# Optimization experiments

Hardware: AMD Instinct MI355X
Metric: run time of the kernel (lower is better)

## Reference

```python
import jax, jax.numpy as jnp
import numpy as np

B, NQ, N, D, H, R = 8, 64, 257, 768, 6, 64
DH = D // H  # 128
ALL_Q_MID = NQ * R  # 4096
LN_EPS = 1e-5


def setup_inputs() -> dict:
    key = jax.random.key(0)
    ks = jax.random.split(key, 7)
    s = 0.02
    return {
        "x": jax.random.normal(ks[0], (B, NQ, D), jnp.float32),
        "context": jax.random.normal(ks[1], (B, N, D), jnp.float32),
        "Wq": jax.random.normal(ks[2], (D, D), jnp.float32) * s,
        "Wk": jax.random.normal(ks[3], (D, D), jnp.float32) * s,
        "Wv1": jax.random.normal(ks[4], (ALL_Q_MID, D), jnp.float32) * s,
        "ln_g": jnp.ones((ALL_Q_MID,), jnp.float32),
        "ln_b": jnp.zeros((ALL_Q_MID,), jnp.float32),
        "Wconv": jax.random.normal(ks[5], (NQ, D, R), jnp.float32) * s,
        "Wout": jax.random.normal(ks[6], (D, D), jnp.float32) * s,
    }


def reference(x, context, Wq, Wk, Wv1, ln_g, ln_b, Wconv, Wout):
    b, nq, d = x.shape
    n = context.shape[1]
    dh = d // H

    # q, k projections, split heads: (b, h, len, dh)
    q = (x @ Wq.T).reshape(b, nq, H, dh).transpose(0, 2, 1, 3)
    k = (context @ Wk.T).reshape(b, n, H, dh).transpose(0, 2, 1, 3)

    # q-aware V: Linear -> LayerNorm(all_q_mid) -> grouped 1x1 conv (per-query lora expand)
    mid = context @ Wv1.T                                   # (b, n, NQ*R)
    mu = mid.mean(-1, keepdims=True)
    var = mid.var(-1, keepdims=True)
    mid = (mid - mu) * jax.lax.rsqrt(var + LN_EPS) * ln_g + ln_b
    midq = mid.reshape(b, n, NQ, -1)                        # (b, n, Q, r)
    v = jnp.einsum('bnqr,qdr->bqnd', midq, Wconv)           # per-query V: (b, Q, n, d)
    v = v.reshape(b, NQ, n, H, dh).transpose(0, 3, 1, 2, 4)  # (b, h, Q, n, dh)

    scale = dh ** (-0.25)
    sim = jnp.einsum('bhid,bhjd->bhij', q * scale, k * scale)  # (b, h, Q, n)
    attn = jax.nn.softmax(sim, axis=-1)
    # per-query value aggregation: attn[i, j] pairs with v[i, j, :]
    out = jnp.einsum('bhij,bhijd->bhid', attn, v)           # (b, h, Q, dh)
    out = out.transpose(0, 2, 1, 3).reshape(b, nq, d)       # (b, Q, d)
    return out @ Wout.T
```

## Files before the change

kernel.cpp:

```cpp
#include <hip/hip_runtime.h>

#define DEV __device__ __forceinline__

typedef __attribute__((ext_vector_type(8))) short sv8;
typedef __attribute__((ext_vector_type(4))) short sv4;
typedef __attribute__((ext_vector_type(4))) float f32x4;

DEV short f2bf(float f) {
  unsigned u = __float_as_uint(f);
  unsigned r = (u + 0x7fffu + ((u >> 16) & 1u)) >> 16;
  return (short)r;
}
DEV float bf2f(short s) {
  return __uint_as_float(((unsigned)(unsigned short)s) << 16);
}

DEV void gload16(const void* g, void* l) {
  __builtin_amdgcn_global_load_lds((const __attribute__((address_space(1))) void*)g,
                                   (__attribute__((address_space(3))) void*)l, 16, 0, 0);
}

struct CvtArgs {
  const float* s0; const float* s1; const float* s2;
  const float* s3; const float* s4; const float* s5;
  short* d0; short* d1; short* d2; short* d3; short* d4; short* d5;
  int e0, e1, e2, e3, e4, e5;
};
__global__ __launch_bounds__(256) void cvt_all(CvtArgs a) {
  int i = blockIdx.x * 256 + threadIdx.x;
  if (i >= a.e5) return;
  const float* s; short* d; int base;
  if      (i < a.e0) { s = a.s0; d = a.d0; base = 0; }
  else if (i < a.e1) { s = a.s1; d = a.d1; base = a.e0; }
  else if (i < a.e2) { s = a.s2; d = a.d2; base = a.e1; }
  else if (i < a.e3) { s = a.s3; d = a.d3; base = a.e2; }
  else if (i < a.e4) { s = a.s4; d = a.d4; base = a.e3; }
  else               { s = a.s5; d = a.d5; base = a.e4; }
  int j = i - base;
  float4 v = ((const float4*)s)[j];
  sv4 o = { f2bf(v.x), f2bf(v.y), f2bf(v.z), f2bf(v.w) };
  ((sv4*)d)[j] = o;
}

template <int OUT_BF16>
DEV void gemm_tile(const short* __restrict__ A, const short* __restrict__ B,
                   void* __restrict__ C, int M, int N, int K, int bm, int bn) {
  __shared__ __align__(16) short As[128 * 32];
  __shared__ __align__(16) short Bs[128 * 32];
  const int tid = threadIdx.x;
  const int wave = tid >> 6, lane = tid & 63;
  const int wr = wave >> 1, wc = wave & 1;
  const int row0 = bm * 128, col0 = bn * 128;
  const int rsel = lane & 15, koff = (lane >> 4) * 8;
  const int Am = M - 1, Bm = N - 1;
  const int lr = lane >> 2, c8 = (lane & 3) * 8;

  const f32x4 z = {0.f, 0.f, 0.f, 0.f};
  f32x4 acc[4][4];
#pragma unroll
  for (int m = 0; m < 4; ++m)
#pragma unroll
    for (int n = 0; n < 4; ++n) acc[m][n] = z;

  for (int k0 = 0; k0 < K; k0 += 32) {
#pragma unroll
    for (int s = 0; s < 2; ++s) {
      int chunk = s * 4 + wave;
      int rr = chunk * 16 + lr;
      int gr = row0 + rr; if (gr > Am) gr = Am;
      gload16(A + (size_t)gr * K + k0 + c8, As + chunk * 512);
      int gc = col0 + rr; if (gc > Bm) gc = Bm;
      gload16(B + (size_t)gc * K + k0 + c8, Bs + chunk * 512);
    }
    __syncthreads();
    sv8 a[4], b[4];
#pragma unroll
    for (int m = 0; m < 4; ++m) a[m] = *(const sv8*)(As + (wr * 64 + m * 16 + rsel) * 32 + koff);
#pragma unroll
    for (int n = 0; n < 4; ++n) b[n] = *(const sv8*)(Bs + (wc * 64 + n * 16 + rsel) * 32 + koff);
#pragma unroll
    for (int m = 0; m < 4; ++m)
#pragma unroll
      for (int n = 0; n < 4; ++n)
        acc[m][n] = __builtin_amdgcn_mfma_f32_16x16x32_bf16(a[m], b[n], acc[m][n], 0, 0, 0);
    __syncthreads();
  }

  const int cc = lane & 15, cr = (lane >> 4) * 4;
#pragma unroll
  for (int m = 0; m < 4; ++m)
#pragma unroll
    for (int n = 0; n < 4; ++n) {
      int c = col0 + wc * 64 + n * 16 + cc;
#pragma unroll
      for (int j = 0; j < 4; ++j) {
        int r = row0 + wr * 64 + m * 16 + cr + j;
        if (r < M && c < N) {
          float v = acc[m][n][j];
          if (OUT_BF16) ((short*)C)[(size_t)r * N + c] = f2bf(v);
          else          ((float*)C)[(size_t)r * N + c] = v;
        }
      }
    }
}

struct GSeg { const short* A; const short* B; short* C; int M; int nb; int blk0; };
__global__ __launch_bounds__(256) void gemm3(GSeg g0, GSeg g1, GSeg g2) {
  int bid = blockIdx.x;
  GSeg g;
  if (bid < g1.blk0) g = g0;
  else if (bid < g2.blk0) g = g1;
  else g = g2;
  int local = bid - g.blk0;
  int bm = local / g.nb, bn = local % g.nb;
  gemm_tile<1>(g.A, g.B, g.C, g.M, g.nb * 128, 768, bm, bn);
}

__global__ __launch_bounds__(256) void gemm_out_k(const short* __restrict__ A,
                                                  const short* __restrict__ B,
                                                  float* __restrict__ C) {
  gemm_tile<0>(A, B, C, 512, 768, 768, blockIdx.x, blockIdx.y);
}

DEV void ln_body(int row, short* __restrict__ mid, const float* __restrict__ g,
                 const float* __restrict__ bb, float* rs, float* rss) {
  short* p = mid + (size_t)row * 4096;
  const int tid = threadIdx.x;
  sv8 v0 = *(const sv8*)(p + tid * 16);
  sv8 v1 = *(const sv8*)(p + tid * 16 + 8);
  float x[16];
#pragma unroll
  for (int j = 0; j < 8; ++j) { x[j] = bf2f(v0[j]); x[8 + j] = bf2f(v1[j]); }
  float s = 0.f, ss = 0.f;
#pragma unroll
  for (int j = 0; j < 16; ++j) { s += x[j]; ss += x[j] * x[j]; }
#pragma unroll
  for (int off = 32; off; off >>= 1) { s += __shfl_xor(s, off); ss += __shfl_xor(ss, off); }
  if ((tid & 63) == 0) { rs[tid >> 6] = s; rss[tid >> 6] = ss; }
  __syncthreads();
  float S = rs[0] + rs[1] + rs[2] + rs[3];
  float SS = rss[0] + rss[1] + rss[2] + rss[3];
  const float inv_n = 1.0f / 4096.0f;
  float mu = S * inv_n;
  float var = SS * inv_n - mu * mu;
  float rstd = rsqrtf(var + 1e-5f);
  const float4* g4 = (const float4*)(g + tid * 16);
  const float4* b4 = (const float4*)(bb + tid * 16);
  float y[16];
#pragma unroll
  for (int i = 0; i < 4; ++i) {
    float4 gg = g4[i], bv = b4[i];
    y[i * 4 + 0] = (x[i * 4 + 0] - mu) * rstd * gg.x + bv.x;
    y[i * 4 + 1] = (x[i * 4 + 1] - mu) * rstd * gg.y + bv.y;
    y[i * 4 + 2] = (x[i * 4 + 2] - mu) * rstd * gg.z + bv.z;
    y[i * 4 + 3] = (x[i * 4 + 3] - mu) * rstd * gg.w + bv.w;
  }
  sv8 o0, o1;
#pragma unroll
  for (int j = 0; j < 8; ++j) { o0[j] = f2bf(y[j]); o1[j] = f2bf(y[8 + j]); }
  *(sv8*)(p + tid * 16) = o0;
  *(sv8*)(p + tid * 16 + 8) = o1;
}

DEV void attn_body(int bh, const short* __restrict__ qb, const short* __restrict__ kb,
                   float* __restrict__ attn, float (*wred)[64]) {
  const int b = bh / 6, h = bh % 6;
  const int tid = threadIdx.x, wave = tid >> 6, lane = tid & 63;
  const int rsel = lane & 15, koff = (lane >> 4) * 8;
  const int rhi = (lane >> 4) * 4;

  const f32x4 z = {0.f, 0.f, 0.f, 0.f};
  f32x4 acc[4][5];
#pragma unroll
  for (int m = 0; m < 4; ++m)
#pragma unroll
    for (int i = 0; i < 5; ++i) acc[m][i] = z;

#pragma unroll
  for (int k0 = 0; k0 < 128; k0 += 32) {
    sv8 a[4];
#pragma unroll
    for (int m = 0; m < 4; ++m)
      a[m] = *(const sv8*)(qb + (size_t)(b * 64 + m * 16 + rsel) * 768 + h * 128 + k0 + koff);
#pragma unroll
    for (int i = 0; i < 5; ++i) {
      int nf = wave + i * 4;
      if (nf > 16) continue;
      int j = nf * 16 + rsel; if (j > 256) j = 256;
      sv8 bf = *(const sv8*)(kb + (size_t)(b * 257 + j) * 768 + h * 128 + k0 + koff);
#pragma unroll
      for (int m = 0; m < 4; ++m)
        acc[m][i] = __builtin_amdgcn_mfma_f32_16x16x32_bf16(a[m], bf, acc[m][i], 0, 0, 0);
    }
  }
  const float S2 = 0.08838834764831845f;
#pragma unroll
  for (int m = 0; m < 4; ++m)
#pragma unroll
    for (int i = 0; i < 5; ++i) {
      int col = (wave + i * 4) * 16 + rsel;
      bool valid = col < 257;
#pragma unroll
      for (int j = 0; j < 4; ++j)
        acc[m][i][j] = valid ? acc[m][i][j] * S2 : -1e30f;
    }
  float mx[4][4];
#pragma unroll
  for (int m = 0; m < 4; ++m)
#pragma unroll
    for (int j = 0; j < 4; ++j) {
      float pm = acc[m][0][j];
#pragma unroll
      for (int i = 1; i < 5; ++i) pm = fmaxf(pm, acc[m][i][j]);
      pm = fmaxf(pm, __shfl_xor(pm, 1));
      pm = fmaxf(pm, __shfl_xor(pm, 2));
      pm = fmaxf(pm, __shfl_xor(pm, 4));
      pm = fmaxf(pm, __shfl_xor(pm, 8));
      mx[m][j] = pm;
      if (rsel == 0) wred[wave][m * 16 + rhi + j] = pm;
    }
  __syncthreads();
#pragma unroll
  for (int m = 0; m < 4; ++m)
#pragma unroll
    for (int j = 0; j < 4; ++j) {
      int row = m * 16 + rhi + j;
      mx[m][j] = fmaxf(fmaxf(wred[0][row], wred[1][row]), fmaxf(wred[2][row], wred[3][row]));
    }
  __syncthreads();
  float inv[4][4];
#pragma unroll
  for (int m = 0; m < 4; ++m)
#pragma unroll
    for (int j = 0; j < 4; ++j) {
      float ps = 0.f;
#pragma unroll
      for (int i = 0; i < 5; ++i) {
        float e = __expf(acc[m][i][j] - mx[m][j]);
        acc[m][i][j] = e;
        ps += e;
      }
      ps += __shfl_xor(ps, 1);
      ps += __shfl_xor(ps, 2);
      ps += __shfl_xor(ps, 4);
      ps += __shfl_xor(ps, 8);
      if (rsel == 0) wred[wave][m * 16 + rhi + j] = ps;
    }
  __syncthreads();
  float* base = attn + (size_t)bh * 64 * 257;
#pragma unroll
  for (int m = 0; m < 4; ++m)
#pragma unroll
    for (int j = 0; j < 4; ++j) {
      int row = m * 16 + rhi + j;
      float tot = wred[0][row] + wred[1][row] + wred[2][row] + wred[3][row];
      inv[m][j] = 1.f / tot;
    }
#pragma unroll
  for (int m = 0; m < 4; ++m)
#pragma unroll
    for (int i = 0; i < 5; ++i) {
      int nf = wave + i * 4;
      if (nf > 16) continue;
      int col = nf * 16 + rsel;
      if (col < 257) {
#pragma unroll
        for (int j = 0; j < 4; ++j)
          base[(size_t)(m * 16 + rhi + j) * 257 + col] = acc[m][i][j] * inv[m][j];
      }
    }
}

__global__ __launch_bounds__(256) void ln_attn(short* __restrict__ mid,
                                               const float* __restrict__ g,
                                               const float* __restrict__ bb,
                                               const short* __restrict__ qb,
                                               const short* __restrict__ kb,
                                               float* __restrict__ attn) {
  __shared__ float wred[4][64];
  __shared__ float rs[4], rss[4];
  if (blockIdx.x < 48) attn_body(blockIdx.x, qb, kb, attn, wred);
  else                 ln_body(blockIdx.x - 48, mid, g, bb, rs, rss);
}

__global__ __launch_bounds__(256) void tk_kernel(const float* __restrict__ attn,
                                                 const short* __restrict__ mid,
                                                 float* __restrict__ t) {
  const int bq = blockIdx.x;
  const int b = bq >> 6, q = bq & 63;
  const int tid = threadIdx.x;
  __shared__ short ms[257][64];
  __shared__ float as_[6][257];
  for (int lin = tid; lin < 257 * 8; lin += 256) {
    int j = lin >> 3, seg = (lin & 7) * 8;
    *(sv8*)(&ms[j][seg]) = *(const sv8*)(mid + (size_t)(b * 257 + j) * 4096 + q * 64 + seg);
  }
#pragma unroll
  for (int h = 0; h < 6; ++h)
    for (int j = tid; j < 257; j += 256)
      as_[h][j] = attn[((size_t)(b * 6 + h) * 64 + q) * 257 + j];
  __syncthreads();
  for (int idx = tid; idx < 384; idx += 256) {
    int h = idx >> 6, r = idx & 63;
    float s = 0.f;
#pragma unroll 4
    for (int j = 0; j < 257; ++j) s += as_[h][j] * bf2f(ms[j][r]);
    t[((size_t)(b * 6 + h) * 64 + q) * 64 + r] = s;
  }
}

__global__ __launch_bounds__(256) void vproj_kernel(const float* __restrict__ t,
                                                    const float* __restrict__ Wconv,
                                                    short* __restrict__ op) {
  const int q = blockIdx.x, chunk = blockIdx.y;
  const int tid = threadIdx.x;
  __shared__ float ts[48][64];
  for (int lin = tid; lin < 48 * 64; lin += 256) {
    int bh = lin >> 6, r = lin & 63;
    ts[bh][r] = t[((size_t)bh * 64 + q) * 64 + r];
  }
  __syncthreads();
  const int d = chunk * 256 + tid;
  const int h = d >> 7;
  const float4* w4 = (const float4*)(Wconv + ((size_t)q * 768 + d) * 64);
  float acc[8] = {0.f, 0.f, 0.f, 0.f, 0.f, 0.f, 0.f, 0.f};
#pragma unroll
  for (int r4 = 0; r4 < 16; ++r4) {
    float4 w = w4[r4];
#pragma unroll
    for (int bb = 0; bb < 8; ++bb) {
      acc[bb] += w.x * ts[bb * 6 + h][r4 * 4 + 0];
      acc[bb] += w.y * ts[bb * 6 + h][r4 * 4 + 1];
      acc[bb] += w.z * ts[bb * 6 + h][r4 * 4 + 2];
      acc[bb] += w.w * ts[bb * 6 + h][r4 * 4 + 3];
    }
  }
#pragma unroll
  for (int bb = 0; bb < 8; ++bb)
    op[((size_t)(bb * 64 + q)) * 768 + d] = f2bf(acc[bb]);
}

extern "C" void kernel_launch(void* const* d_in, const int* in_sizes, int n_in,
                              void* d_out, int out_size, void* d_ws, size_t ws_size,
                              hipStream_t stream) {
  const float* x = (const float*)d_in[0];
  const float* ctx = (const float*)d_in[1];
  const float* Wq = (const float*)d_in[2];
  const float* Wk = (const float*)d_in[3];
  const float* Wv1 = (const float*)d_in[4];
  const float* ln_g = (const float*)d_in[5];
  const float* ln_b = (const float*)d_in[6];
  const float* Wconv = (const float*)d_in[7];
  const float* Wout = (const float*)d_in[8];
  float* out = (float*)d_out;
  (void)in_sizes; (void)n_in; (void)out_size; (void)ws_size;

  char* ws = (char*)d_ws;
  size_t off = 0;
  auto alloc = [&](size_t bytes) -> void* {
    void* p = (void*)(ws + off);
    off += (bytes + 255) & ~(size_t)255;
    return p;
  };
  short* x_bf    = (short*)alloc((size_t)393216 * 2);
  short* ctx_bf  = (short*)alloc((size_t)1579008 * 2);
  short* wq_bf   = (short*)alloc((size_t)589824 * 2);
  short* wk_bf   = (short*)alloc((size_t)589824 * 2);
  short* wv1_bf  = (short*)alloc((size_t)3145728 * 2);
  short* wout_bf = (short*)alloc((size_t)589824 * 2);
  short* q_bf    = (short*)alloc((size_t)393216 * 2);
  short* k_bf    = (short*)alloc((size_t)1579008 * 2);
  short* mid_bf  = (short*)alloc((size_t)8421376 * 2);
  float* attn    = (float*)alloc((size_t)789504 * 4);
  float* tbuf    = (float*)alloc((size_t)196608 * 4);
  short* op_bf   = (short*)alloc((size_t)393216 * 2);

  CvtArgs ca;
  ca.s0 = x;   ca.d0 = x_bf;    int n0 = 393216 / 4;
  ca.s1 = ctx; ca.d1 = ctx_bf;  int n1 = 1579008 / 4;
  ca.s2 = Wq;  ca.d2 = wq_bf;   int n2 = 589824 / 4;
  ca.s3 = Wk;  ca.d3 = wk_bf;   int n3 = 589824 / 4;
  ca.s4 = Wv1; ca.d4 = wv1_bf;  int n4 = 3145728 / 4;
  ca.s5 = Wout; ca.d5 = wout_bf; int n5 = 589824 / 4;
  ca.e0 = n0; ca.e1 = ca.e0 + n1; ca.e2 = ca.e1 + n2;
  ca.e3 = ca.e2 + n3; ca.e4 = ca.e3 + n4; ca.e5 = ca.e4 + n5;
  cvt_all<<<dim3((ca.e5 + 255) / 256), dim3(256), 0, stream>>>(ca);

  GSeg s_q   = { x_bf,   wq_bf,  q_bf,   512,  6, 0 };
  GSeg s_k   = { ctx_bf, wk_bf,  k_bf,   2056, 6, 24 };
  GSeg s_mid = { ctx_bf, wv1_bf, mid_bf, 2056, 32, 126 };
  gemm3<<<dim3(670), dim3(256), 0, stream>>>(s_q, s_k, s_mid);

  ln_attn<<<dim3(2104), dim3(256), 0, stream>>>(mid_bf, ln_g, ln_b, q_bf, k_bf, attn);

  tk_kernel<<<dim3(512), dim3(256), 0, stream>>>(attn, mid_bf, tbuf);

  vproj_kernel<<<dim3(64, 3), dim3(256), 0, stream>>>(tbuf, Wconv, op_bf);

  gemm_out_k<<<dim3(4, 6), dim3(256), 0, stream>>>(op_bf, wout_bf, out);
}
```

Measured before the change: 188.3 us.

## Double-buffer GEMM LDS tiles, swizzle layout, split-K the output projection

```diff
diff --git a/kernel.cpp b/kernel.cpp
--- a/kernel.cpp
+++ b/kernel.cpp
@@ -18,6 +18,11 @@
 DEV void gload16(const void* g, void* l) {
   __builtin_amdgcn_global_load_lds((const __attribute__((address_space(1))) void*)g,
                                    (__attribute__((address_space(3))) void*)l, 16, 0, 0);
+}
+
+__global__ __launch_bounds__(256) void fill_zero(float* __restrict__ p, int n4) {
+  int i = blockIdx.x * 256 + threadIdx.x;
+  if (i < n4) ((float4*)p)[i] = make_float4(0.f, 0.f, 0.f, 0.f);
 }
 
 struct CvtArgs {
@@ -42,18 +47,23 @@
   ((sv4*)d)[j] = o;
 }
 
-template <int OUT_BF16>
+template <int MODE, int SPLITK>
 DEV void gemm_tile(const short* __restrict__ A, const short* __restrict__ B,
-                   void* __restrict__ C, int M, int N, int K, int bm, int bn) {
-  __shared__ __align__(16) short As[128 * 32];
-  __shared__ __align__(16) short Bs[128 * 32];
+                   void* __restrict__ C, int M, int N, int K,
+                   int bm, int bn, int ks) {
+  __shared__ __align__(16) short As[2][4096];
+  __shared__ __align__(16) short Bs[2][4096];
   const int tid = threadIdx.x;
   const int wave = tid >> 6, lane = tid & 63;
   const int wr = wave >> 1, wc = wave & 1;
   const int row0 = bm * 128, col0 = bn * 128;
-  const int rsel = lane & 15, koff = (lane >> 4) * 8;
+  const int rsel = lane & 15;
   const int Am = M - 1, Bm = N - 1;
-  const int lr = lane >> 2, c8 = (lane & 3) * 8;
+  const int lr = lane >> 2;
+  const int c8 = ((lane & 3) ^ ((lane >> 2) & 3)) * 8;
+  const int Ksl = K / SPLITK;
+  const int kbase = ks * Ksl;
+  const int nt = Ksl / 32;
 
   const f32x4 z = {0.f, 0.f, 0.f, 0.f};
   f32x4 acc[4][4];
@@ -62,22 +72,33 @@
 #pragma unroll
     for (int n = 0; n < 4; ++n) acc[m][n] = z;
 
-  for (int k0 = 0; k0 < K; k0 += 32) {
+  auto stage = [&](int t, int buf) {
+    int k0 = kbase + t * 32;
 #pragma unroll
     for (int s = 0; s < 2; ++s) {
       int chunk = s * 4 + wave;
       int rr = chunk * 16 + lr;
       int gr = row0 + rr; if (gr > Am) gr = Am;
-      gload16(A + (size_t)gr * K + k0 + c8, As + chunk * 512);
+      gload16(A + (size_t)gr * K + k0 + c8, &As[buf][chunk * 512]);
       int gc = col0 + rr; if (gc > Bm) gc = Bm;
-      gload16(B + (size_t)gc * K + k0 + c8, Bs + chunk * 512);
-    }
-    __syncthreads();
+      gload16(B + (size_t)gc * K + k0 + c8, &Bs[buf][chunk * 512]);
+    }
+  };
+
+  stage(0, 0);
+  __syncthreads();
+  const int ko = (((lane >> 4) ^ (rsel & 3)) * 8);
+
+  for (int t = 0; t < nt; ++t) {
+    int cur = t & 1;
+    if (t + 1 < nt) stage(t + 1, cur ^ 1);
     sv8 a[4], b[4];
 #pragma unroll
-    for (int m = 0; m < 4; ++m) a[m] = *(const sv8*)(As + (wr * 64 + m * 16 + rsel) * 32 + koff);
-#pragma unroll
-    for (int n = 0; n < 4; ++n) b[n] = *(const sv8*)(Bs + (wc * 64 + n * 16 + rsel) * 32 + koff);
+    for (int m = 0; m < 4; ++m)
+      a[m] = *(const sv8*)(&As[cur][(wr * 64 + m * 16 + rsel) * 32 + ko]);
+#pragma unroll
+    for (int n = 0; n < 4; ++n)
+      b[n] = *(const sv8*)(&Bs[cur][(wc * 64 + n * 16 + rsel) * 32 + ko]);
 #pragma unroll
     for (int m = 0; m < 4; ++m)
 #pragma unroll
@@ -97,8 +118,9 @@
         int r = row0 + wr * 64 + m * 16 + cr + j;
         if (r < M && c < N) {
           float v = acc[m][n][j];
-          if (OUT_BF16) ((short*)C)[(size_t)r * N + c] = f2bf(v);
-          else          ((float*)C)[(size_t)r * N + c] = v;
+          if (MODE == 1)      ((short*)C)[(size_t)r * N + c] = f2bf(v);
+          else if (MODE == 0) ((float*)C)[(size_t)r * N + c] = v;
+          else                atomicAdd(&((float*)C)[(size_t)r * N + c], v);
         }
       }
     }
@@ -113,13 +135,13 @@
   else g = g2;
   int local = bid - g.blk0;
   int bm = local / g.nb, bn = local % g.nb;
-  gemm_tile<1>(g.A, g.B, g.C, g.M, g.nb * 128, 768, bm, bn);
+  gemm_tile<1, 1>(g.A, g.B, g.C, g.M, g.nb * 128, 768, bm, bn, 0);
 }
 
 __global__ __launch_bounds__(256) void gemm_out_k(const short* __restrict__ A,
                                                   const short* __restrict__ B,
                                                   float* __restrict__ C) {
-  gemm_tile<0>(A, B, C, 512, 768, 768, blockIdx.x, blockIdx.y);
+  gemm_tile<2, 4>(A, B, C, 512, 768, 768, blockIdx.x, blockIdx.y, blockIdx.z);
 }
 
 DEV void ln_body(int row, short* __restrict__ mid, const float* __restrict__ g,
@@ -375,6 +397,8 @@
   float* tbuf    = (float*)alloc((size_t)196608 * 4);
   short* op_bf   = (short*)alloc((size_t)393216 * 2);
 
+  fill_zero<<<dim3(384), dim3(256), 0, stream>>>(out, 393216 / 4);
+
   CvtArgs ca;
   ca.s0 = x;   ca.d0 = x_bf;    int n0 = 393216 / 4;
   ca.s1 = ctx; ca.d1 = ctx_bf;  int n1 = 1579008 / 4;
@@ -397,5 +421,5 @@
 
   vproj_kernel<<<dim3(64, 3), dim3(256), 0, stream>>>(tbuf, Wconv, op_bf);
 
-  gemm_out_k<<<dim3(4, 6), dim3(256), 0, stream>>>(op_bf, wout_bf, out);
-}
+  gemm_out_k<<<dim3(4, 6, 4), dim3(256), 0, stream>>>(op_bf, wout_bf, out);
+}
```

Measured after the change: 183.5 us. 2.5% less time.
